# Kernel optimization log

Hardware: AMD Instinct MI355X
Metric: run time of the kernel (lower is better)

The kernel has to match this reference:

```python
import jax, jax.numpy as jnp
import numpy as np

B, S, DM, H = 2, 2048, 1024, 16
HD = DM // H


def setup_inputs() -> dict:
    key = jax.random.key(0)
    ks = jax.random.split(key, 12)
    xavier = lambda k: jax.random.uniform(k, (DM, DM), jnp.float32,
                                          -np.sqrt(6.0 / (DM + DM)), np.sqrt(6.0 / (DM + DM)))
    return {
        "q": jax.random.normal(ks[0], (B, S, DM), jnp.float32),
        "k": jax.random.normal(ks[1], (B, S, DM), jnp.float32),
        "v": jax.random.normal(ks[2], (B, S, DM), jnp.float32),
        "mask": jnp.ones((B, S, S), jnp.int32),
        "Wq": xavier(ks[3]), "bq": jnp.zeros((DM,), jnp.float32),
        "Wk": xavier(ks[4]), "bk": jnp.zeros((DM,), jnp.float32),
        "Wv": xavier(ks[5]), "bv": jnp.zeros((DM,), jnp.float32),
        "Wf": xavier(ks[6]), "bf": jnp.zeros((DM,), jnp.float32),
    }


def reference(q, k, v, mask, Wq, bq, Wk, bk, Wv, bv, Wf, bf):
    b, s, dm = q.shape
    # projections (torch Linear: x @ W.T + b)
    qh = (q @ Wq.T + bq).reshape(b, s, H, HD).transpose(0, 2, 1, 3)  # [B,H,S,HD]
    kh = (k @ Wk.T + bk).reshape(b, -1, H, HD).transpose(0, 2, 1, 3)
    vh = (v @ Wv.T + bv).reshape(b, -1, H, HD).transpose(0, 2, 1, 3)
    scores = jnp.einsum('bhqd,bhkd->bhqk', qh, kh) / np.sqrt(HD)    # [B,H,S,S]
    scores = jnp.where(mask[:, None, :, :] == 0, -jnp.inf, scores)
    attn = jax.nn.softmax(scores, axis=-1)
    out = jnp.einsum('bhqk,bhkd->bhqd', attn, vh)                   # [B,H,S,HD]
    out = out.transpose(0, 2, 1, 3).reshape(b, s, dm)
    return out @ Wf.T + bf, attn
```

## Files before the change

kernel.cpp:

```cpp
#include <hip/hip_runtime.h>
#include <stdint.h>


typedef _Float16 f16x8 __attribute__((ext_vector_type(8)));
typedef __fp16 fp16v2 __attribute__((ext_vector_type(2)));
typedef float f32x4 __attribute__((ext_vector_type(4)));
typedef unsigned long long ull;

static_assert(sizeof(f16x8) == 16, "f16x8 must be 16B");

#define MFMA16(a, b, c) __builtin_amdgcn_mfma_f32_16x16x32_f16((a), (b), (c), 0, 0, 0)

__device__ __forceinline__ unsigned short f2h_(float f) {
  _Float16 h = (_Float16)f;
  return __builtin_bit_cast(unsigned short, h);
}

__device__ __forceinline__ unsigned pk2_(float a, float b) {
  fp16v2 h = __builtin_amdgcn_cvt_pkrtz(a, b);
  return __builtin_bit_cast(unsigned, h);
}

__global__ __launch_bounds__(256) void cvt_kernel(
    const float* __restrict__ q, const float* __restrict__ k,
    const float* __restrict__ v, const float* __restrict__ wq,
    const float* __restrict__ wk, const float* __restrict__ wv,
    const float* __restrict__ wf, unsigned short* __restrict__ dst) {
  long e0 = ((long)blockIdx.x * 256 + threadIdx.x) * 8;
  const float* src; long off;
  if (e0 < 4194304L)       { src = q;  off = e0; }
  else if (e0 < 8388608L)  { src = k;  off = e0 - 4194304L; }
  else if (e0 < 12582912L) { src = v;  off = e0 - 8388608L; }
  else if (e0 < 13631488L) { src = wq; off = e0 - 12582912L; }
  else if (e0 < 14680064L) { src = wk; off = e0 - 13631488L; }
  else if (e0 < 15728640L) { src = wv; off = e0 - 14680064L; }
  else                     { src = wf; off = e0 - 15728640L; }
  float4 a = *(const float4*)(src + off);
  float4 b = *(const float4*)(src + off + 4);
  uint4 o;
  o.x = (unsigned)f2h_(a.x) | ((unsigned)f2h_(a.y) << 16);
  o.y = (unsigned)f2h_(a.z) | ((unsigned)f2h_(a.w) << 16);
  o.z = (unsigned)f2h_(b.x) | ((unsigned)f2h_(b.y) << 16);
  o.w = (unsigned)f2h_(b.z) | ((unsigned)f2h_(b.w) << 16);
  *(uint4*)(dst + e0) = o;
}

__global__ __launch_bounds__(256) void mask_pack(const int* __restrict__ mask,
                                                 ull* __restrict__ mb) {
  int wid = (int)((blockIdx.x * 256 + threadIdx.x) >> 6);
  int lane = threadIdx.x & 63;
  int nw = (int)((gridDim.x * 256) >> 6);
  for (int w = wid; w < 131072; w += nw) {
    int val = mask[(long)w * 64 + lane];
    ull bits = __ballot(val != 0);
    if (lane == 0) mb[w] = bits;
  }
}

__device__ __forceinline__ void gemm_body(
    const unsigned short* __restrict__ A, const unsigned short* __restrict__ Bm,
    const float* __restrict__ bias, unsigned short* __restrict__ outb,
    float* __restrict__ outf, int mode) {
  __shared__ unsigned short Al[128 * 64];
  __shared__ unsigned short Bl[128 * 64];
  const int tid = threadIdx.x, lane = tid & 63, wave = tid >> 6;
  const int lo = lane & 15, hi = lane >> 4;
  const int wi = wave >> 1, wj = wave & 1;
  const int ib = blockIdx.y << 7, jb = blockIdx.x << 7;
  const int cb0 = hi << 4;
  f32x4 acc[4][4] = {};
  for (int kt = 0; kt < 16; ++kt) {
    const int k0 = kt << 6;
    __syncthreads();
#pragma unroll
    for (int i = 0; i < 4; ++i) {
      int u = tid + (i << 8), r = u >> 3, c = u & 7;
      uint4 av = *(const uint4*)(A + (long)(ib + r) * 1024 + k0 + c * 8);
      uint4 bv = *(const uint4*)(Bm + (long)(jb + r) * 1024 + k0 + c * 8);
      *(uint4*)((char*)Al + r * 128 + ((c * 16) ^ ((r & 7) << 4))) = av;
      *(uint4*)((char*)Bl + r * 128 + ((c * 16) ^ ((r & 7) << 4))) = bv;
    }
    __syncthreads();
    f16x8 af[4][2], bfr[4][2];
#pragma unroll
    for (int it = 0; it < 4; ++it) {
      int r = (wi << 6) + (it << 4) + lo;
      af[it][0] = *(const f16x8*)((char*)Al + r * 128 + (cb0 ^ ((r & 7) << 4)));
      af[it][1] = *(const f16x8*)((char*)Al + r * 128 + ((64 + cb0) ^ ((r & 7) << 4)));
    }
#pragma unroll
    for (int jt = 0; jt < 4; ++jt) {
      int r = (wj << 6) + (jt << 4) + lo;
      bfr[jt][0] = *(const f16x8*)((char*)Bl + r * 128 + (cb0 ^ ((r & 7) << 4)));
      bfr[jt][1] = *(const f16x8*)((char*)Bl + r * 128 + ((64 + cb0) ^ ((r & 7) << 4)));
    }
#pragma unroll
    for (int it = 0; it < 4; ++it)
#pragma unroll
      for (int jt = 0; jt < 4; ++jt) {
        acc[it][jt] = MFMA16(af[it][0], bfr[jt][0], acc[it][jt]);
        acc[it][jt] = MFMA16(af[it][1], bfr[jt][1], acc[it][jt]);
      }
  }
#pragma unroll
  for (int it = 0; it < 4; ++it)
#pragma unroll
    for (int jt = 0; jt < 4; ++jt) {
      f32x4 vv = acc[it][jt];
      int i0 = ib + (wi << 6) + (it << 4) + (hi << 2);
      int j = jb + (wj << 6) + (jt << 4) + lo;
      float4 bb = *(const float4*)(bias + i0);
      vv[0] += bb.x; vv[1] += bb.y; vv[2] += bb.z; vv[3] += bb.w;
      if (mode == 2) {
        float4 st; st.x = vv[0]; st.y = vv[1]; st.z = vv[2]; st.w = vv[3];
        *(float4*)(outf + (long)j * 1024 + i0) = st;
      } else {
        int h = i0 >> 6, dd = i0 & 63, b2 = j >> 11, s2 = j & 2047;
        if (mode == 0) {
          ull pk = (ull)f2h_(vv[0]) | ((ull)f2h_(vv[1]) << 16) |
                   ((ull)f2h_(vv[2]) << 32) | ((ull)f2h_(vv[3]) << 48);
          *(ull*)(outb + ((long)((b2 * 16 + h) * 2048 + s2)) * 64 + dd) = pk;
        } else {
          unsigned short* p = outb + ((long)((b2 * 16 + h) * 64 + dd)) * 2048 + s2;
          p[0] = f2h_(vv[0]); p[2048] = f2h_(vv[1]);
          p[4096] = f2h_(vv[2]); p[6144] = f2h_(vv[3]);
        }
      }
    }
}

__global__ __launch_bounds__(256) void gemm_qkv(
    const unsigned short* __restrict__ xb, const float* __restrict__ bq,
    const float* __restrict__ bk, const float* __restrict__ bv,
    unsigned short* __restrict__ outbase) {
  const int z = blockIdx.z;
  const unsigned short* A = xb + 12582912 + (long)z * 1048576;
  const unsigned short* Bm = xb + (long)z * 4194304;
  const float* bias = (z == 0) ? bq : ((z == 1) ? bk : bv);
  unsigned short* outp = outbase + (long)z * 4194304;
  gemm_body(A, Bm, bias, outp, nullptr, (z == 2) ? 1 : 0);
}

__global__ __launch_bounds__(256) void gemm_f(
    const unsigned short* __restrict__ xb, const unsigned short* __restrict__ oh,
    const float* __restrict__ bias, float* __restrict__ outf) {
  gemm_body(xb + 15728640, oh, bias, nullptr, outf, 2);
}

__global__ __launch_bounds__(256, 3) void attn_kernel(
    const unsigned short* __restrict__ qh, const unsigned short* __restrict__ kh,
    const unsigned short* __restrict__ vt, const ull* __restrict__ mb,
    float* __restrict__ attnp, unsigned short* __restrict__ oh) {
  __shared__ unsigned short Ks[128 * 64];
  __shared__ unsigned short Vs[64 * 128];
  __shared__ unsigned short Ps[64 * 128];
  const int tid = threadIdx.x, lane = tid & 63, wave = tid >> 6;
  const int lo = lane & 15, hi = lane >> 4;
  const int cb0 = hi << 4;
  int id = blockIdx.x;
  int wgid = (id & 7) * 128 + (id >> 3);
  const int bh = wgid >> 5, b_ = bh >> 4;
  const int q0 = (wgid & 31) << 6;
  const float cs = 0.18033688011112042f;

  const int rq = (wave << 4) + lo;
  const int qg = q0 + rq;
  const int swq = (rq & 7) << 4;
  const unsigned short* qp = qh + ((long)bh * 2048 + qg) * 64;
  f16x8 aq0 = *(const f16x8*)(qp + (hi << 3));
  f16x8 aq1 = *(const f16x8*)(qp + 32 + (hi << 3));
  const ull* mrow = mb + (long)(b_ * 2048 + qg) * 32;

  float ll = 0.f;
  f32x4 oacc[4] = {};

  for (int kt = 0; kt < 16; ++kt) {
    __syncthreads();
#pragma unroll
    for (int i = 0; i < 4; ++i) {
      int u = tid + (i << 8);
      { int r = u >> 3, c = u & 7;
        uint4 d = *(const uint4*)(kh + ((long)bh * 2048 + (kt << 7) + r) * 64 + c * 8);
        *(uint4*)((char*)Ks + r * 128 + ((c * 16) ^ ((r & 7) << 4))) = d; }
      { int r = u >> 4, c = u & 15;
        uint4 d = *(const uint4*)(vt + ((long)bh * 64 + r) * 2048 + (kt << 7) + c * 8);
        *(uint4*)((char*)Vs + r * 256 + ((c * 16) ^ ((r & 7) << 4))) = d; }
    }
    __syncthreads();
    f32x4 fa[8];
#pragma unroll
    for (int nt = 0; nt < 8; ++nt) {
      int rk = (nt << 4) + lo;
      int swk = (rk & 7) << 4;
      f16x8 k0 = *(const f16x8*)((char*)Ks + rk * 128 + (cb0 ^ swk));
      f16x8 k1 = *(const f16x8*)((char*)Ks + rk * 128 + ((64 + cb0) ^ swk));
      f32x4 z = {};
      z = MFMA16(k0, aq0, z);
      z = MFMA16(k1, aq1, z);
      fa[nt] = z;
    }
    ull mw0 = mrow[(kt << 1)], mw1 = mrow[(kt << 1) + 1];
    const bool fast = __all((int)((mw0 & mw1) == ~0ull));
#pragma unroll
    for (int nt = 0; nt < 8; ++nt) {
      float e0 = __builtin_amdgcn_exp2f(fa[nt][0] * cs);
      float e1 = __builtin_amdgcn_exp2f(fa[nt][1] * cs);
      float e2 = __builtin_amdgcn_exp2f(fa[nt][2] * cs);
      float e3 = __builtin_amdgcn_exp2f(fa[nt][3] * cs);
      if (!fast) {
        int kb = (nt << 4) + (hi << 2);
        ull mws = (kb & 64) ? mw1 : mw0;
        int sh = kb & 63;
        if (!((mws >> sh) & 1ull)) e0 = 0.f;
        if (!((mws >> (sh + 1)) & 1ull)) e1 = 0.f;
        if (!((mws >> (sh + 2)) & 1ull)) e2 = 0.f;
        if (!((mws >> (sh + 3)) & 1ull)) e3 = 0.f;
      }
      ll += (e0 + e1) + (e2 + e3);
      ull pk = (ull)pk2_(e0, e1) | ((ull)pk2_(e2, e3) << 32);
      *(ull*)((char*)Ps + rq * 256 + (((nt << 5) + (hi << 3)) ^ swq)) = pk;
    }
    f16x8 ap[4];
#pragma unroll
    for (int ks = 0; ks < 4; ++ks)
      ap[ks] = *(const f16x8*)((char*)Ps + rq * 256 + (((ks << 6) + cb0) ^ swq));
#pragma unroll
    for (int nt = 0; nt < 4; ++nt) {
      int rv = (nt << 4) + lo;
      int swv = (rv & 7) << 4;
#pragma unroll
      for (int ks = 0; ks < 4; ++ks) {
        f16x8 bvv = *(const f16x8*)((char*)Vs + rv * 256 + (((ks << 6) + cb0) ^ swv));
        oacc[nt] = MFMA16(ap[ks], bvv, oacc[nt]);
      }
    }
  }
  ll += __shfl_xor(ll, 16);
  ll += __shfl_xor(ll, 32);
  const float rl = (ll > 0.f) ? (1.f / ll) : 0.f;
  const float lrl = __log2f(rl);

  float rlr[4];
#pragma unroll
  for (int r = 0; r < 4; ++r) rlr[r] = __shfl(rl, (hi << 2) + r, 16);
#pragma unroll
  for (int nt = 0; nt < 4; ++nt)
#pragma unroll
    for (int r = 0; r < 4; ++r) {
      int qe = q0 + (wave << 4) + (hi << 2) + r;
      oh[(long)(b_ * 2048 + qe) * 1024 + ((bh & 15) << 6) + (nt << 4) + lo] =
          f2h_(oacc[nt][r] * rlr[r]);
    }

  float* arow = attnp + ((long)bh * 2048 + qg) * 2048;
  for (int kt = 0; kt < 16; ++kt) {
    __syncthreads();
#pragma unroll
    for (int i = 0; i < 4; ++i) {
      int u = tid + (i << 8), r = u >> 3, c = u & 7;
      uint4 d = *(const uint4*)(kh + ((long)bh * 2048 + (kt << 7) + r) * 64 + c * 8);
      *(uint4*)((char*)Ks + r * 128 + ((c * 16) ^ ((r & 7) << 4))) = d;
    }
    __syncthreads();
    f32x4 fa[8];
#pragma unroll
    for (int nt = 0; nt < 8; ++nt) {
      int rk = (nt << 4) + lo;
      int swk = (rk & 7) << 4;
      f16x8 k0 = *(const f16x8*)((char*)Ks + rk * 128 + (cb0 ^ swk));
      f16x8 k1 = *(const f16x8*)((char*)Ks + rk * 128 + ((64 + cb0) ^ swk));
      f32x4 z = {};
      z = MFMA16(k0, aq0, z);
      z = MFMA16(k1, aq1, z);
      fa[nt] = z;
    }
    ull mw0 = mrow[(kt << 1)], mw1 = mrow[(kt << 1) + 1];
    const bool fast = __all((int)((mw0 & mw1) == ~0ull));
#pragma unroll
    for (int nt = 0; nt < 8; ++nt) {
      float e0 = __builtin_amdgcn_exp2f(fa[nt][0] * cs + lrl);
      float e1 = __builtin_amdgcn_exp2f(fa[nt][1] * cs + lrl);
      float e2 = __builtin_amdgcn_exp2f(fa[nt][2] * cs + lrl);
      float e3 = __builtin_amdgcn_exp2f(fa[nt][3] * cs + lrl);
      if (!fast) {
        int kb = (nt << 4) + (hi << 2);
        ull mws = (kb & 64) ? mw1 : mw0;
        int sh = kb & 63;
        if (!((mws >> sh) & 1ull)) e0 = 0.f;
        if (!((mws >> (sh + 1)) & 1ull)) e1 = 0.f;
        if (!((mws >> (sh + 2)) & 1ull)) e2 = 0.f;
        if (!((mws >> (sh + 3)) & 1ull)) e3 = 0.f;
      }
      f32x4 st; st[0] = e0; st[1] = e1; st[2] = e2; st[3] = e3;
      __builtin_nontemporal_store(st, (f32x4*)(arow + (kt << 7) + (nt << 4) + (hi << 2)));
    }
  }
}

extern "C" void kernel_launch(void* const* d_in, const int* in_sizes, int n_in,
                              void* d_out, int out_size, void* d_ws, size_t ws_size,
                              hipStream_t stream) {
  const float* q = (const float*)d_in[0];
  const float* k = (const float*)d_in[1];
  const float* v = (const float*)d_in[2];
  const int* mask = (const int*)d_in[3];
  const float* Wq = (const float*)d_in[4];
  const float* bq = (const float*)d_in[5];
  const float* Wk = (const float*)d_in[6];
  const float* bk = (const float*)d_in[7];
  const float* Wv = (const float*)d_in[8];
  const float* bv = (const float*)d_in[9];
  const float* Wf = (const float*)d_in[10];
  const float* bf_ = (const float*)d_in[11];

  float* out = (float*)d_out;
  float* attn = out + 4194304;

  unsigned short* xb = (unsigned short*)d_ws;
  unsigned short* qhp = xb + 16777216;
  unsigned short* khp = qhp + 4194304;
  unsigned short* vtp = khp + 4194304;
  unsigned short* ohp = vtp + 4194304;
  ull* mb = (ull*)((char*)d_ws + 67108864);

  cvt_kernel<<<dim3(8192), dim3(256), 0, stream>>>(q, k, v, Wq, Wk, Wv, Wf, xb);
  mask_pack<<<dim3(512), dim3(256), 0, stream>>>(mask, mb);
  gemm_qkv<<<dim3(32, 8, 3), dim3(256), 0, stream>>>(xb, bq, bk, bv, qhp);
  attn_kernel<<<dim3(1024), dim3(256), 0, stream>>>(qhp, khp, vtp, mb, attn, ohp);
  gemm_f<<<dim3(32, 8), dim3(256), 0, stream>>>(xb, ohp, bf_, out);
}
```

Measured before the change: 311.1 us.

## Double-buffer K/V tiles in attention and merge conversion with mask packing

In the attention kernel, K and V tiles now live in two shared-memory buffers, so the next tile is loaded while the current one is computed, replacing the two barriers per iteration with one. The occupancy hint drops from 3 to 2 workgroups per CU to make room for the larger shared-memory footprint. The float-to-half conversion and mask packing kernels are fused into one launch, and conversion now uses packed cvt_pkrtz, which rounds toward zero instead of to nearest. The risks are lower occupancy and a slight change in rounding.

Measured after the change: 293.7 us. -5.6%, faster.

```diff
diff --git a/kernel.cpp b/kernel.cpp
--- a/kernel.cpp
+++ b/kernel.cpp
@@ -21,39 +21,39 @@
   return __builtin_bit_cast(unsigned, h);
 }
 
-__global__ __launch_bounds__(256) void cvt_kernel(
+__global__ __launch_bounds__(256) void prep_kernel(
     const float* __restrict__ q, const float* __restrict__ k,
     const float* __restrict__ v, const float* __restrict__ wq,
     const float* __restrict__ wk, const float* __restrict__ wv,
-    const float* __restrict__ wf, unsigned short* __restrict__ dst) {
-  long e0 = ((long)blockIdx.x * 256 + threadIdx.x) * 8;
-  const float* src; long off;
-  if (e0 < 4194304L)       { src = q;  off = e0; }
-  else if (e0 < 8388608L)  { src = k;  off = e0 - 4194304L; }
-  else if (e0 < 12582912L) { src = v;  off = e0 - 8388608L; }
-  else if (e0 < 13631488L) { src = wq; off = e0 - 12582912L; }
-  else if (e0 < 14680064L) { src = wk; off = e0 - 13631488L; }
-  else if (e0 < 15728640L) { src = wv; off = e0 - 14680064L; }
-  else                     { src = wf; off = e0 - 15728640L; }
-  float4 a = *(const float4*)(src + off);
-  float4 b = *(const float4*)(src + off + 4);
-  uint4 o;
-  o.x = (unsigned)f2h_(a.x) | ((unsigned)f2h_(a.y) << 16);
-  o.y = (unsigned)f2h_(a.z) | ((unsigned)f2h_(a.w) << 16);
-  o.z = (unsigned)f2h_(b.x) | ((unsigned)f2h_(b.y) << 16);
-  o.w = (unsigned)f2h_(b.z) | ((unsigned)f2h_(b.w) << 16);
-  *(uint4*)(dst + e0) = o;
-}
-
-__global__ __launch_bounds__(256) void mask_pack(const int* __restrict__ mask,
-                                                 ull* __restrict__ mb) {
-  int wid = (int)((blockIdx.x * 256 + threadIdx.x) >> 6);
-  int lane = threadIdx.x & 63;
-  int nw = (int)((gridDim.x * 256) >> 6);
-  for (int w = wid; w < 131072; w += nw) {
-    int val = mask[(long)w * 64 + lane];
-    ull bits = __ballot(val != 0);
-    if (lane == 0) mb[w] = bits;
+    const float* __restrict__ wf, unsigned short* __restrict__ dst,
+    const int* __restrict__ mask, ull* __restrict__ mb) {
+  int bid = blockIdx.x;
+  if (bid < 8192) {
+    long e0 = ((long)bid * 256 + threadIdx.x) * 8;
+    const float* src; long off;
+    if (e0 < 4194304L)       { src = q;  off = e0; }
+    else if (e0 < 8388608L)  { src = k;  off = e0 - 4194304L; }
+    else if (e0 < 12582912L) { src = v;  off = e0 - 8388608L; }
+    else if (e0 < 13631488L) { src = wq; off = e0 - 12582912L; }
+    else if (e0 < 14680064L) { src = wk; off = e0 - 13631488L; }
+    else if (e0 < 15728640L) { src = wv; off = e0 - 14680064L; }
+    else                     { src = wf; off = e0 - 15728640L; }
+    float4 a = *(const float4*)(src + off);
+    float4 b = *(const float4*)(src + off + 4);
+    uint4 o;
+    o.x = pk2_(a.x, a.y);
+    o.y = pk2_(a.z, a.w);
+    o.z = pk2_(b.x, b.y);
+    o.w = pk2_(b.z, b.w);
+    *(uint4*)(dst + e0) = o;
+  } else {
+    int wid = (int)(((bid - 8192) * 256 + threadIdx.x) >> 6);
+    int lane = threadIdx.x & 63;
+    for (int w = wid; w < 131072; w += 2048) {
+      int val = mask[(long)w * 64 + lane];
+      ull bits = __ballot(val != 0);
+      if (lane == 0) mb[w] = bits;
+    }
   }
 }
 
@@ -147,12 +147,12 @@
   gemm_body(xb + 15728640, oh, bias, nullptr, outf, 2);
 }
 
-__global__ __launch_bounds__(256, 3) void attn_kernel(
+__global__ __launch_bounds__(256, 2) void attn_kernel(
     const unsigned short* __restrict__ qh, const unsigned short* __restrict__ kh,
     const unsigned short* __restrict__ vt, const ull* __restrict__ mb,
     float* __restrict__ attnp, unsigned short* __restrict__ oh) {
-  __shared__ unsigned short Ks[128 * 64];
-  __shared__ unsigned short Vs[64 * 128];
+  __shared__ unsigned short Ks[2][128 * 64];
+  __shared__ unsigned short Vs[2][64 * 128];
   __shared__ unsigned short Ps[64 * 128];
   const int tid = threadIdx.x, lane = tid & 63, wave = tid >> 6;
   const int lo = lane & 15, hi = lane >> 4;
@@ -170,30 +170,44 @@
   f16x8 aq0 = *(const f16x8*)(qp + (hi << 3));
   f16x8 aq1 = *(const f16x8*)(qp + 32 + (hi << 3));
   const ull* mrow = mb + (long)(b_ * 2048 + qg) * 32;
+  const unsigned short* khb = kh + (long)bh * 2048 * 64;
+  const unsigned short* vtb = vt + (long)bh * 64 * 2048;
 
   float ll = 0.f;
   f32x4 oacc[4] = {};
 
+#define STAGE_KV(KT, BUF)                                                      \
+  _Pragma("unroll") for (int i = 0; i < 4; ++i) {                              \
+    int u = tid + (i << 8);                                                    \
+    { int r = u >> 3, c = u & 7;                                               \
+      uint4 d = *(const uint4*)(khb + (long)(((KT) << 7) + r) * 64 + c * 8);   \
+      *(uint4*)((char*)Ks[BUF] + r * 128 + ((c * 16) ^ ((r & 7) << 4))) = d; } \
+    { int r = u >> 4, c = u & 15;                                              \
+      uint4 d = *(const uint4*)(vtb + (long)r * 2048 + ((KT) << 7) + c * 8);   \
+      *(uint4*)((char*)Vs[BUF] + r * 256 + ((c * 16) ^ ((r & 7) << 4))) = d; } \
+  }
+
+#define STAGE_K(KT, BUF)                                                       \
+  _Pragma("unroll") for (int i = 0; i < 4; ++i) {                              \
+    int u = tid + (i << 8), r = u >> 3, c = u & 7;                             \
+    uint4 d = *(const uint4*)(khb + (long)(((KT) << 7) + r) * 64 + c * 8);     \
+    *(uint4*)((char*)Ks[BUF] + r * 128 + ((c * 16) ^ ((r & 7) << 4))) = d;     \
+  }
+
+  STAGE_KV(0, 0);
+  __syncthreads();
   for (int kt = 0; kt < 16; ++kt) {
-    __syncthreads();
-#pragma unroll
-    for (int i = 0; i < 4; ++i) {
-      int u = tid + (i << 8);
-      { int r = u >> 3, c = u & 7;
-        uint4 d = *(const uint4*)(kh + ((long)bh * 2048 + (kt << 7) + r) * 64 + c * 8);
-        *(uint4*)((char*)Ks + r * 128 + ((c * 16) ^ ((r & 7) << 4))) = d; }
-      { int r = u >> 4, c = u & 15;
-        uint4 d = *(const uint4*)(vt + ((long)bh * 64 + r) * 2048 + (kt << 7) + c * 8);
-        *(uint4*)((char*)Vs + r * 256 + ((c * 16) ^ ((r & 7) << 4))) = d; }
-    }
-    __syncthreads();
+    const int cur = kt & 1;
+    if (kt < 15) STAGE_KV(kt + 1, cur ^ 1);
+    const unsigned short* Kc = Ks[cur];
+    const unsigned short* Vc = Vs[cur];
     f32x4 fa[8];
 #pragma unroll
     for (int nt = 0; nt < 8; ++nt) {
       int rk = (nt << 4) + lo;
       int swk = (rk & 7) << 4;
-      f16x8 k0 = *(const f16x8*)((char*)Ks + rk * 128 + (cb0 ^ swk));
-      f16x8 k1 = *(const f16x8*)((char*)Ks + rk * 128 + ((64 + cb0) ^ swk));
+      f16x8 k0 = *(const f16x8*)((const char*)Kc + rk * 128 + (cb0 ^ swk));
+      f16x8 k1 = *(const f16x8*)((const char*)Kc + rk * 128 + ((64 + cb0) ^ swk));
       f32x4 z = {};
       z = MFMA16(k0, aq0, z);
       z = MFMA16(k1, aq1, z);
@@ -230,10 +244,11 @@
       int swv = (rv & 7) << 4;
 #pragma unroll
       for (int ks = 0; ks < 4; ++ks) {
-        f16x8 bvv = *(const f16x8*)((char*)Vs + rv * 256 + (((ks << 6) + cb0) ^ swv));
+        f16x8 bvv = *(const f16x8*)((const char*)Vc + rv * 256 + (((ks << 6) + cb0) ^ swv));
         oacc[nt] = MFMA16(ap[ks], bvv, oacc[nt]);
       }
     }
+    __syncthreads();
   }
   ll += __shfl_xor(ll, 16);
   ll += __shfl_xor(ll, 32);
@@ -253,22 +268,19 @@
     }
 
   float* arow = attnp + ((long)bh * 2048 + qg) * 2048;
+  STAGE_K(0, 0);
+  __syncthreads();
   for (int kt = 0; kt < 16; ++kt) {
-    __syncthreads();
-#pragma unroll
-    for (int i = 0; i < 4; ++i) {
-      int u = tid + (i << 8), r = u >> 3, c = u & 7;
-      uint4 d = *(const uint4*)(kh + ((long)bh * 2048 + (kt << 7) + r) * 64 + c * 8);
-      *(uint4*)((char*)Ks + r * 128 + ((c * 16) ^ ((r & 7) << 4))) = d;
-    }
-    __syncthreads();
+    const int cur = kt & 1;
+    if (kt < 15) STAGE_K(kt + 1, cur ^ 1);
+    const unsigned short* Kc = Ks[cur];
     f32x4 fa[8];
 #pragma unroll
     for (int nt = 0; nt < 8; ++nt) {
       int rk = (nt << 4) + lo;
       int swk = (rk & 7) << 4;
-      f16x8 k0 = *(const f16x8*)((char*)Ks + rk * 128 + (cb0 ^ swk));
-      f16x8 k1 = *(const f16x8*)((char*)Ks + rk * 128 + ((64 + cb0) ^ swk));
+      f16x8 k0 = *(const f16x8*)((const char*)Kc + rk * 128 + (cb0 ^ swk));
+      f16x8 k1 = *(const f16x8*)((const char*)Kc + rk * 128 + ((64 + cb0) ^ swk));
       f32x4 z = {};
       z = MFMA16(k0, aq0, z);
       z = MFMA16(k1, aq1, z);
@@ -294,6 +306,7 @@
       f32x4 st; st[0] = e0; st[1] = e1; st[2] = e2; st[3] = e3;
       __builtin_nontemporal_store(st, (f32x4*)(arow + (kt << 7) + (nt << 4) + (hi << 2)));
     }
+    __syncthreads();
   }
 }
 
@@ -323,8 +336,8 @@
   unsigned short* ohp = vtp + 4194304;
   ull* mb = (ull*)((char*)d_ws + 67108864);
 
-  cvt_kernel<<<dim3(8192), dim3(256), 0, stream>>>(q, k, v, Wq, Wk, Wv, Wf, xb);
-  mask_pack<<<dim3(512), dim3(256), 0, stream>>>(mask, mb);
+  prep_kernel<<<dim3(8704), dim3(256), 0, stream>>>(q, k, v, Wq, Wk, Wv, Wf, xb,
+                                                    mask, mb);
   gemm_qkv<<<dim3(32, 8, 3), dim3(256), 0, stream>>>(xb, bq, bk, bv, qhp);
   attn_kernel<<<dim3(1024), dim3(256), 0, stream>>>(qhp, khp, vtp, mb, attn, ohp);
   gemm_f<<<dim3(32, 8), dim3(256), 0, stream>>>(xb, ohp, bf_, out);
```
